# Optimization experiments

Measured on AMD Instinct MI355X. Metric: run time of the kernel, lower is better.

Reference implementation:

```python
import jax, jax.numpy as jnp
import numpy as np

B, IMGS, PH, PW = 4, 4, 16, 16      # 4 groups, 4 images/group, 16x16 patches per image
P, C = 16, 3
N = IMGS * PH * PW                   # 1024 packed tokens per group
PATCH_DIM = C * P * P                # 768
DIM, HEADS, DHEAD, DEPTH = 768, 12, 64, 4
INNER = HEADS * DHEAD
MLP = 3072
POSMAX = 32                          # image_size // patch_size
NCLS = 1000
SCALE = DHEAD ** 0.5


def _ln(x, g):
    # torch LayerNorm with learned gamma, beta frozen at 0
    mu = jnp.mean(x, -1, keepdims=True)
    var = jnp.var(x, -1, keepdims=True)
    return (x - mu) * jax.lax.rsqrt(var + 1e-5) * g


def _qk_rmsnorm(t, g):
    # F.normalize(t, dim=-1) * sqrt(dhead) * gamma[h, 1, d]; t: (b,h,n,d), g: (h,d)
    nrm = jnp.sqrt(jnp.sum(t * t, -1, keepdims=True))
    return t / jnp.maximum(nrm, 1e-12) * SCALE * g[None, :, None, :]


def _attention(x, context, ln_g, Wq, Wkv, qg, kg, Wo, attn_mask):
    xn = _ln(x, ln_g)
    kv_in = xn if context is None else context  # context is NOT normed (matches torch)
    q = xn @ Wq
    k, v = jnp.split(kv_in @ Wkv, 2, axis=-1)
    split = lambda t: t.reshape(t.shape[0], t.shape[1], HEADS, DHEAD).transpose(0, 2, 1, 3)
    q, k, v = split(q), split(k), split(v)
    q = _qk_rmsnorm(q, qg)
    k = _qk_rmsnorm(k, kg)
    dots = jnp.einsum('bhid,bhjd->bhij', q, k)  # no 1/sqrt(d): scale lives in RMSNorm
    dots = jnp.where(attn_mask, dots, -jnp.finfo(dots.dtype).max)
    attn = jax.nn.softmax(dots, axis=-1)
    out = jnp.einsum('bhij,bhjd->bhid', attn, v)
    out = out.transpose(0, 2, 1, 3).reshape(x.shape[0], -1, INNER)
    return out @ Wo


def _forward(patches, emb_ln_g, W_emb, b_emb, emb_ln2_g, pos_h, pos_w,
             ln_attn_g, Wq, Wkv, qn_g, kn_g, Wo,
             ln_ff_g, W1, b1, W2, b2, final_ln_g,
             pool_q, pool_ln_g, pWq, pWkv, p_qn_g, p_kn_g, pWo,
             head_ln_g, W_head,
             patch_positions, image_ids, lengths):
    valid = jnp.arange(N)[None, :] < lengths[:, None]              # (B,N) True = real token
    same_img = image_ids[:, :, None] == image_ids[:, None, :]      # (B,i,j) block-diagonal
    attn_mask = (same_img & valid[:, None, :])[:, None]            # (B,1,i,j)

    x = _ln(patches, emb_ln_g) @ W_emb + b_emb
    x = _ln(x, emb_ln2_g)
    x = x + pos_h[patch_positions[..., 0]] + pos_w[patch_positions[..., 1]]

    for l in range(DEPTH):
        x = _attention(x, None, ln_attn_g[l], Wq[l], Wkv[l], qn_g[l], kn_g[l], Wo[l], attn_mask) + x
        h = jax.nn.gelu(_ln(x, ln_ff_g[l]) @ W1[l] + b1[l], approximate=False)
        x = h @ W2[l] + b2[l] + x
    x = _ln(x, final_ln_g)

    # attention pooling: one learned query per packed image
    queries = jnp.broadcast_to(pool_q, (x.shape[0], IMGS, DIM))
    pool_mask = ((jnp.arange(IMGS)[None, :, None] == image_ids[:, None, :]) & valid[:, None, :])[:, None]
    pooled = _attention(queries, x, pool_ln_g, pWq, pWkv, p_qn_g, p_kn_g, pWo, pool_mask) + queries
    return _ln(pooled, head_ln_g) @ W_head  # (B, IMGS, NCLS), mlp_head has no bias


def setup_inputs():
    key = jax.random.key(0)
    ks = jax.random.split(key, 20)
    rn = lambda k, shape, s=0.02: (jax.random.normal(k, shape) * s).astype(jnp.float32)

    patches = jax.random.normal(ks[0], (B, N, PATCH_DIM), dtype=jnp.float32)
    hh, ww = jnp.meshgrid(jnp.arange(PH), jnp.arange(PW), indexing='ij')
    pos = jnp.stack([hh.reshape(-1), ww.reshape(-1)], axis=-1)        # (256,2)
    patch_positions = jnp.broadcast_to(jnp.tile(pos, (IMGS, 1))[None], (B, N, 2)).astype(jnp.int32)
    image_ids = jnp.broadcast_to(jnp.repeat(jnp.arange(IMGS), PH * PW)[None], (B, N)).astype(jnp.int32)
    lengths = jnp.full((B,), N, dtype=jnp.int32)

    return dict(
        patches=patches, patch_positions=patch_positions, image_ids=image_ids, lengths=lengths,
        emb_ln_g=jnp.ones(PATCH_DIM, jnp.float32), W_emb=rn(ks[1], (PATCH_DIM, DIM)),
        b_emb=jnp.zeros(DIM, jnp.float32), emb_ln2_g=jnp.ones(DIM, jnp.float32),
        pos_h=rn(ks[2], (POSMAX, DIM), 1.0), pos_w=rn(ks[3], (POSMAX, DIM), 1.0),
        ln_attn_g=jnp.ones((DEPTH, DIM), jnp.float32),
        Wq=rn(ks[4], (DEPTH, DIM, INNER)), Wkv=rn(ks[5], (DEPTH, DIM, 2 * INNER)),
        qn_g=jnp.ones((DEPTH, HEADS, DHEAD), jnp.float32), kn_g=jnp.ones((DEPTH, HEADS, DHEAD), jnp.float32),
        Wo=rn(ks[6], (DEPTH, INNER, DIM)),
        ln_ff_g=jnp.ones((DEPTH, DIM), jnp.float32),
        W1=rn(ks[7], (DEPTH, DIM, MLP)), b1=jnp.zeros((DEPTH, MLP), jnp.float32),
        W2=rn(ks[8], (DEPTH, MLP, DIM)), b2=jnp.zeros((DEPTH, DIM), jnp.float32),
        final_ln_g=jnp.ones(DIM, jnp.float32),
        pool_q=rn(ks[9], (DIM,), 1.0), pool_ln_g=jnp.ones(DIM, jnp.float32),
        pWq=rn(ks[10], (DIM, INNER)), pWkv=rn(ks[11], (DIM, 2 * INNER)),
        p_qn_g=jnp.ones((HEADS, DHEAD), jnp.float32), p_kn_g=jnp.ones((HEADS, DHEAD), jnp.float32),
        pWo=rn(ks[12], (INNER, DIM)),
        head_ln_g=jnp.ones(DIM, jnp.float32), W_head=rn(ks[13], (DIM, NCLS)),
    )


def reference(patches, patch_positions, image_ids, lengths,
              emb_ln_g, W_emb, b_emb, emb_ln2_g, pos_h, pos_w,
              ln_attn_g, Wq, Wkv, qn_g, kn_g, Wo,
              ln_ff_g, W1, b1, W2, b2, final_ln_g,
              pool_q, pool_ln_g, pWq, pWkv, p_qn_g, p_kn_g, pWo,
              head_ln_g, W_head):
    return _forward(patches, emb_ln_g, W_emb, b_emb, emb_ln2_g, pos_h, pos_w,
                    ln_attn_g, Wq, Wkv, qn_g, kn_g, Wo,
                    ln_ff_g, W1, b1, W2, b2, final_ln_g,
                    pool_q, pool_ln_g, pWq, pWkv, p_qn_g, p_kn_g, pWo,
                    head_ln_g, W_head, patch_positions, image_ids, lengths)
```

## Files before the change

### kernel.cpp

```cpp
#include <hip/hip_runtime.h>
#include <hip/hip_bf16.h>
#include <math.h>

using bf16 = __hip_bfloat16;
typedef short s16x8 __attribute__((ext_vector_type(8)));
typedef float f32x4 __attribute__((ext_vector_type(4)));

#define DEVI __device__ __forceinline__

static constexpr int NB    = 4;
static constexpr int NTOK  = 1024;
static constexpr int DIM   = 768;
static constexpr int NH    = 12;
static constexpr int MLPD  = 3072;
static constexpr int NLAYER= 4;
static constexpr int NIMG  = 4;
static constexpr int NCLS  = 1000;
static constexpr int MR    = NB * NTOK;

DEVI float b2f(bf16 v){ return __bfloat162float(v); }
DEVI bf16  f2b(float v){ return __float2bfloat16(v); }

DEVI void async16(const void* g, void* l) {
  __builtin_amdgcn_global_load_lds((const __attribute__((address_space(1))) void*)g,
                                   (__attribute__((address_space(3))) void*)l, 16, 0, 0);
}

DEVI f32x4 mfma16(s16x8 a, s16x8 b, f32x4 c) {
  return __builtin_amdgcn_mfma_f32_16x16x32_bf16(a, b, c, 0, 0, 0);
}

template<int N> DEVI void waitcnt_vm() {
  if constexpr (N == 0)      asm volatile("s_waitcnt vmcnt(0)" ::: "memory");
  else if constexpr (N == 4) asm volatile("s_waitcnt vmcnt(4)" ::: "memory");
  else if constexpr (N == 6) asm volatile("s_waitcnt vmcnt(6)" ::: "memory");
}

DEVI float block_sum(float v, float* scratch, int tid) {
  #pragma unroll
  for (int o = 32; o >= 1; o >>= 1) v += __shfl_xor(v, o);
  __syncthreads();
  if ((tid & 63) == 0) scratch[tid >> 6] = v;
  __syncthreads();
  return scratch[0] + scratch[1] + scratch[2] + scratch[3];
}

DEVI float block_max(float v, float* scratch, int tid) {
  #pragma unroll
  for (int o = 32; o >= 1; o >>= 1) v = fmaxf(v, __shfl_xor(v, o));
  __syncthreads();
  if ((tid & 63) == 0) scratch[tid >> 6] = v;
  __syncthreads();
  return fmaxf(fmaxf(scratch[0], scratch[1]), fmaxf(scratch[2], scratch[3]));
}

struct bh4 { bf16 a, b, c, d; };
struct TEntry { const float* src; bf16* dst; int R, C, tiles, tC; };
struct TDesc  { TEntry e[22]; };

__global__ __launch_bounds__(256) void transpose_kernel(TDesc D, int nent) {
  int bid = blockIdx.x, ei = 0;
  while (ei < nent - 1 && bid >= D.e[ei].tiles) { bid -= D.e[ei].tiles; ++ei; }
  const TEntry E = D.e[ei];
  const int tr = bid / E.tC, tc = bid % E.tC;
  __shared__ bf16 t[32][33];
  const int tid = threadIdx.x;
  const int lr = tid >> 3, lc = (tid & 7) * 4;
  const float* srow = E.src + (size_t)(tr*32 + lr)*E.C + tc*32 + lc;
  float4 v = *(const float4*)srow;
  t[lr][lc] = f2b(v.x); t[lr][lc+1] = f2b(v.y); t[lr][lc+2] = f2b(v.z); t[lr][lc+3] = f2b(v.w);
  __syncthreads();
  bh4 o;
  o.a = t[lc+0][lr]; o.b = t[lc+1][lr]; o.c = t[lc+2][lr]; o.d = t[lc+3][lr];
  *(bh4*)(E.dst + (size_t)(tc*32 + lr)*E.R + tr*32 + lc) = o;
}

__global__ __launch_bounds__(256) void ln768_kernel(const float* __restrict__ in,
    const float* __restrict__ g, bf16* __restrict__ out)
{
  __shared__ float scratch[4];
  const int row = blockIdx.x, tid = threadIdx.x;
  const float* p = in + (size_t)row*768;
  const float v0 = p[tid], v1 = p[tid+256], v2 = p[tid+512];
  const float s  = block_sum(v0+v1+v2, scratch, tid);
  const float ss = block_sum(v0*v0+v1*v1+v2*v2, scratch, tid);
  const float mu = s * (1.0f/768.0f);
  const float var = ss * (1.0f/768.0f) - mu*mu;
  const float rstd = rsqrtf(var + 1e-5f);
  bf16* o = out + (size_t)row*768;
  o[tid]     = f2b((v0-mu)*rstd*g[tid]);
  o[tid+256] = f2b((v1-mu)*rstd*g[tid+256]);
  o[tid+512] = f2b((v2-mu)*rstd*g[tid+512]);
}

__global__ __launch_bounds__(256) void ln_pos_kernel(const float* __restrict__ in,
    const float* __restrict__ g, const float* __restrict__ pos_h, const float* __restrict__ pos_w,
    const int* __restrict__ ppos, float* __restrict__ out)
{
  __shared__ float scratch[4];
  const int row = blockIdx.x, tid = threadIdx.x;
  const float* p = in + (size_t)row*768;
  const float v0 = p[tid], v1 = p[tid+256], v2 = p[tid+512];
  const float s  = block_sum(v0+v1+v2, scratch, tid);
  const float ss = block_sum(v0*v0+v1*v1+v2*v2, scratch, tid);
  const float mu = s * (1.0f/768.0f);
  const float rstd = rsqrtf(ss*(1.0f/768.0f) - mu*mu + 1e-5f);
  const int p0 = ppos[row*2], p1 = ppos[row*2+1];
  const float* ph = pos_h + (size_t)p0*768;
  const float* pw = pos_w + (size_t)p1*768;
  float* o = out + (size_t)row*768;
  o[tid]     = (v0-mu)*rstd*g[tid]     + ph[tid]     + pw[tid];
  o[tid+256] = (v1-mu)*rstd*g[tid+256] + ph[tid+256] + pw[tid+256];
  o[tid+512] = (v2-mu)*rstd*g[tid+512] + ph[tid+512] + pw[tid+512];
}

template<int DO_BIAS, int DO_GELU, int OUT_BF16, int DO_RES, int NTILE>
__global__ __launch_bounds__(256)
void gemm_mfma(const bf16* __restrict__ A, const bf16* __restrict__ BT,
               const float* __restrict__ bias, float* __restrict__ Cf,
               bf16* __restrict__ Cb, int M, int Nn, int K)
{
  constexpr int NF  = NTILE / 32;
  constexpr int PD  = (NTILE == 64) ? 4 : 3;
  constexpr int VW  = (NTILE == 64) ? 6 : 4;
  __shared__ bf16 As[PD][64*64];
  __shared__ bf16 Bs[PD][(NTILE/2)*64];
  const int tid = threadIdx.x;
  const int wid = tid >> 6, lane = tid & 63;
  const int quad = lane >> 4, l15 = lane & 15;
  const int wy = wid >> 1, wx = wid & 1;

  const int gx  = gridDim.x;
  const int nwg = gx * gridDim.y;
  const int bid = blockIdx.y * gx + blockIdx.x;
  const int qq  = nwg >> 3, rm = nwg & 7;
  const int xcd = bid & 7,  li = bid >> 3;
  const int swz = (xcd < rm ? xcd * (qq + 1) : rm * (qq + 1) + (xcd - rm) * qq) + li;
  const int m0 = (swz / gx) * 128, n0 = (swz % gx) * NTILE;

  const int rl = lane >> 3;
  const int cs = lane & 7;

  f32x4 acc[4][NF];
  #pragma unroll
  for (int i = 0; i < 4; ++i)
    #pragma unroll
    for (int j = 0; j < NF; ++j) acc[i][j] = (f32x4){0.f,0.f,0.f,0.f};

  auto stage = [&](int buf, int k0) {
    #pragma unroll
    for (int c = 0; c < 2; ++c) {
      const int rbase = wid*8 + c*32;
      const int r_abs = rbase + rl;
      const int ceff  = cs ^ (r_abs & 7);
      const int mg    = 2*r_abs + (ceff >> 2);
      const int jb    = (ceff & 3) * 16;
      async16((const char*)A + ((size_t)(m0 + mg)*K + k0)*2 + jb, (char*)As[buf] + rbase*128);
    }
    #pragma unroll
    for (int c = 0; c < NTILE/64; ++c) {
      const int rbase = wid*8 + c*32;
      const int r_abs = rbase + rl;
      const int ceff  = cs ^ (r_abs & 7);
      const int ng    = 2*r_abs + (ceff >> 2);
      const int jb    = (ceff & 3) * 16;
      async16((const char*)BT + ((size_t)(n0 + ng)*K + k0)*2 + jb, (char*)Bs[buf] + rbase*128);
    }
  };

  auto compute = [&](int cb) {
    s16x8 af[4], bfr[NF];
    #pragma unroll
    for (int mt = 0; mt < 4; ++mt) {
      const int m = wy*64 + mt*16 + l15;
      const int r = m >> 1;
      const int cq = (((m & 1) << 2) | quad) ^ (r & 7);
      af[mt] = *(const s16x8*)((const char*)As[cb] + r*128 + cq*16);
    }
    #pragma unroll
    for (int nt = 0; nt < NF; ++nt) {
      const int n = wx*(NTILE/2) + nt*16 + l15;
      const int r = n >> 1;
      const int cq = (((n & 1) << 2) | quad) ^ (r & 7);
      bfr[nt] = *(const s16x8*)((const char*)Bs[cb] + r*128 + cq*16);
    }
    #pragma unroll
    for (int mt = 0; mt < 4; ++mt)
      #pragma unroll
      for (int nt = 0; nt < NF; ++nt)
        acc[mt][nt] = mfma16(af[mt], bfr[nt], acc[mt][nt]);
  };

  const int nk = K >> 5;
  #pragma unroll
  for (int t = 0; t < PD - 1; ++t) stage(t, t << 5);

  int cbuf = 0, sbuf = PD - 1;
  const int mainN = nk - (PD - 1);
  for (int kt = 0; kt < mainN; ++kt) {
    __builtin_amdgcn_sched_barrier(0);
    waitcnt_vm<VW>();
    __builtin_amdgcn_s_barrier();
    __builtin_amdgcn_sched_barrier(0);
    stage(sbuf, (kt + PD - 1) << 5);
    compute(cbuf);
    cbuf = (cbuf + 1 == PD) ? 0 : cbuf + 1;
    sbuf = (sbuf + 1 == PD) ? 0 : sbuf + 1;
  }
  for (int kt = mainN; kt < nk; ++kt) {
    __builtin_amdgcn_sched_barrier(0);
    waitcnt_vm<0>();
    __builtin_amdgcn_s_barrier();
    __builtin_amdgcn_sched_barrier(0);
    compute(cbuf);
    cbuf = (cbuf + 1 == PD) ? 0 : cbuf + 1;
  }

  #pragma unroll
  for (int nt = 0; nt < NF; ++nt) {
    const int col = n0 + wx*(NTILE/2) + nt*16 + l15;
    float bv = 0.f;
    if constexpr (DO_BIAS) bv = bias[col];
    #pragma unroll
    for (int mt = 0; mt < 4; ++mt) {
      #pragma unroll
      for (int r = 0; r < 4; ++r) {
        const int row = m0 + wy*64 + mt*16 + quad*4 + r;
        float v = acc[mt][nt][r];
        if constexpr (DO_BIAS) v += bv;
        if constexpr (DO_GELU) v = 0.5f*v*(1.0f + erff(v*0.70710678118654752f));
        const size_t idx = (size_t)row*Nn + col;
        if constexpr (OUT_BF16) Cb[idx] = f2b(v);
        else if constexpr (DO_RES) Cf[idx] += v;
        else Cf[idx] = v;
      }
    }
  }
}

template<int IN_BF16, int DO_BIAS>
__global__ __launch_bounds__(256) void smallm_gemm(const void* __restrict__ Xv,
    const float* __restrict__ W, const float* __restrict__ bias,
    float* __restrict__ out, int Nn)
{
  __shared__ float Xs[16*768];
  __shared__ float red[4][16][64];
  const int tid = threadIdx.x;
  if constexpr (IN_BF16) {
    const bf16* X = (const bf16*)Xv;
    for (int i = tid; i < 16*768; i += 256) Xs[i] = b2f(X[i]);
  } else {
    const float* X = (const float*)Xv;
    for (int i = tid; i < 16*768; i += 256) Xs[i] = X[i];
  }
  __syncthreads();
  const int cl = tid & 63, kg = tid >> 6;
  const int c = blockIdx.x*64 + cl;
  float acc[16];
  #pragma unroll
  for (int r = 0; r < 16; ++r) acc[r] = 0.f;
  if (c < Nn) {
    const int k0 = kg*192;
    #pragma unroll 4
    for (int k = k0; k < k0 + 192; ++k) {
      const float w = W[(size_t)k*Nn + c];
      #pragma unroll
      for (int r = 0; r < 16; ++r) acc[r] += Xs[r*768 + k] * w;
    }
  }
  #pragma unroll
  for (int r = 0; r < 16; ++r) red[kg][r][cl] = acc[r];
  __syncthreads();
  if (kg == 0 && c < Nn) {
    #pragma unroll
    for (int r = 0; r < 16; ++r) {
      float v = red[0][r][cl] + red[1][r][cl] + red[2][r][cl] + red[3][r][cl];
      if constexpr (DO_BIAS) v += bias[c];
      out[(size_t)r*Nn + c] = v;
    }
  }
}

__global__ __launch_bounds__(256) void rms_qkv_kernel(const float* __restrict__ qkv,
    const float* __restrict__ qg, const float* __restrict__ kg,
    bf16* __restrict__ Qb, bf16* __restrict__ Kb, bf16* __restrict__ VTb)
{
  __shared__ float tile[64*68];
  const int nt = blockIdx.x, h = blockIdx.y, b = blockIdx.z;
  const int tid = threadIdx.x;
  const int bh = b*NH + h;
  const size_t rowbase = (size_t)(b*NTOK + nt*64);
  const int r = tid >> 2, pp = tid & 3;

  auto stage = [&](int off) {
    #pragma unroll
    for (int rr = 0; rr < 4; ++rr) {
      const int idx = rr*256 + tid;
      const int rw = idx >> 4, c4 = (idx & 15) << 2;
      float4 val = *(const float4*)(qkv + (rowbase + rw)*2304 + off + c4);
      *(float4*)(&tile[rw*68 + c4]) = val;
    }
  };

  stage(h*64);
  __syncthreads();
  {
    float ssq = 0.f;
    #pragma unroll
    for (int i = 0; i < 16; ++i) { float x = tile[r*68 + pp*16 + i]; ssq += x*x; }
    ssq += __shfl_xor(ssq, 1); ssq += __shfl_xor(ssq, 2);
    const float rn = 8.0f / fmaxf(sqrtf(ssq), 1e-12f);
    bf16* orow = Qb + ((size_t)bh*NTOK + nt*64 + r)*64;
    #pragma unroll
    for (int i = 0; i < 16; ++i) { int d = pp*16+i; orow[d] = f2b(tile[r*68+d]*rn*qg[h*64+d]); }
  }
  __syncthreads();
  stage(768 + h*64);
  __syncthreads();
  {
    float ssq = 0.f;
    #pragma unroll
    for (int i = 0; i < 16; ++i) { float x = tile[r*68 + pp*16 + i]; ssq += x*x; }
    ssq += __shfl_xor(ssq, 1); ssq += __shfl_xor(ssq, 2);
    const float rn = 8.0f / fmaxf(sqrtf(ssq), 1e-12f);
    bf16* orow = Kb + ((size_t)bh*NTOK + nt*64 + r)*64;
    #pragma unroll
    for (int i = 0; i < 16; ++i) { int d = pp*16+i; orow[d] = f2b(tile[r*68+d]*rn*kg[h*64+d]); }
  }
  __syncthreads();
  stage(1536 + h*64);
  __syncthreads();
  {
    const int d = tid >> 2;
    bf16* orow = VTb + ((size_t)bh*64 + d)*NTOK + nt*64;
    #pragma unroll
    for (int i = 0; i < 16; ++i) { int n = pp*16 + i; orow[n] = f2b(tile[n*68 + d]); }
  }
}

__global__ __launch_bounds__(256) void attn_mfma(const bf16* __restrict__ Qb,
    const bf16* __restrict__ Kb, const bf16* __restrict__ VTb, bf16* __restrict__ Ob,
    const int* __restrict__ ids, const int* __restrict__ lens)
{
  __shared__ bf16 Ps[4][16*72];
  __shared__ int  ids_s[NTOK];
  const int qt = blockIdx.x, h = blockIdx.y, b = blockIdx.z;
  const int tid = threadIdx.x;
  const int wid = tid >> 6, lane = tid & 63;
  const int quad = lane >> 4, l15 = lane & 15;
  const int bh = b*NH + h;
  const int q0 = qt*64;
  const int len = lens[b];

  #pragma unroll
  for (int i = 0; i < 4; ++i) ids_s[i*256 + tid] = ids[b*NTOK + i*256 + tid];
  __syncthreads();

  const bf16* qrow = Qb + ((size_t)bh*NTOK + q0 + wid*16 + l15)*64;
  const s16x8 aq0 = *(const s16x8*)(qrow + quad*8);
  const s16x8 aq1 = *(const s16x8*)(qrow + 32 + quad*8);

  int idq[4];
  #pragma unroll
  for (int rr = 0; rr < 4; ++rr) idq[rr] = ids_s[q0 + wid*16 + quad*4 + rr];

  unsigned qm = 0;
  #pragma unroll
  for (int rr = 0; rr < 4; ++rr) qm |= 1u << (idq[rr] & 31);
  #pragma unroll
  for (int o = 32; o >= 1; o >>= 1) qm |= (unsigned)__shfl_xor((int)qm, o);

  f32x4 oacc[4];
  #pragma unroll
  for (int nt = 0; nt < 4; ++nt) oacc[nt] = (f32x4){0.f,0.f,0.f,0.f};
  float mrow[4] = {-3.0e38f,-3.0e38f,-3.0e38f,-3.0e38f};
  float lrow[4] = {0.f,0.f,0.f,0.f};

  const bf16* Kgb = Kb  + (size_t)bh*NTOK*64;
  const bf16* Vgb = VTb + (size_t)bh*64*NTOK;
  bf16* pw = Ps[wid];

  for (int kt = 0; kt < 16; ++kt) {
    const int k0 = kt*64;
    const int idk_l = ids_s[k0 + lane];
    const bool ok = ((k0 + lane) < len) && (((qm >> (idk_l & 31)) & 1u) != 0u);
    if (__ballot(ok) == 0ULL) continue;

    f32x4 sA[4];
    #pragma unroll
    for (int jt = 0; jt < 4; ++jt) {
      const bf16* krow = Kgb + (size_t)(k0 + jt*16 + l15)*64;
      const s16x8 bk0 = *(const s16x8*)(krow + quad*8);
      const s16x8 bk1 = *(const s16x8*)(krow + 32 + quad*8);
      f32x4 s = (f32x4){0.f,0.f,0.f,0.f};
      s = mfma16(aq0, bk0, s);
      s = mfma16(aq1, bk1, s);
      sA[jt] = s;
    }
    #pragma unroll
    for (int jt = 0; jt < 4; ++jt) {
      const int j = k0 + jt*16 + l15;
      const int idk = ids_s[j];
      const bool kvld = j < len;
      #pragma unroll
      for (int rr = 0; rr < 4; ++rr)
        sA[jt][rr] = (kvld && idk == idq[rr]) ? sA[jt][rr] : -3.0e38f;
    }
    float alpha[4], mnew[4];
    #pragma unroll
    for (int rr = 0; rr < 4; ++rr) {
      float mx = fmaxf(fmaxf(sA[0][rr], sA[1][rr]), fmaxf(sA[2][rr], sA[3][rr]));
      mx = fmaxf(mx, __shfl_xor(mx, 1));
      mx = fmaxf(mx, __shfl_xor(mx, 2));
      mx = fmaxf(mx, __shfl_xor(mx, 4));
      mx = fmaxf(mx, __shfl_xor(mx, 8));
      const float mn = fmaxf(mrow[rr], mx);
      mnew[rr] = mn;
      alpha[rr] = expf(mrow[rr] - mn);
      mrow[rr] = mn;
    }
    #pragma unroll
    for (int rr = 0; rr < 4; ++rr) {
      float rs = 0.f;
      #pragma unroll
      for (int jt = 0; jt < 4; ++jt) {
        const float pv = (sA[jt][rr] > -1.0e38f) ? expf(sA[jt][rr] - mnew[rr]) : 0.0f;
        sA[jt][rr] = pv;
        rs += pv;
      }
      rs += __shfl_xor(rs, 1);
      rs += __shfl_xor(rs, 2);
      rs += __shfl_xor(rs, 4);
      rs += __shfl_xor(rs, 8);
      lrow[rr] = lrow[rr]*alpha[rr] + rs;
      #pragma unroll
      for (int nt = 0; nt < 4; ++nt) oacc[nt][rr] *= alpha[rr];
    }
    #pragma unroll
    for (int jt = 0; jt < 4; ++jt)
      #pragma unroll
      for (int rr = 0; rr < 4; ++rr)
        pw[(quad*4+rr)*72 + jt*16 + l15] = f2b(sA[jt][rr]);
    #pragma unroll
    for (int ss = 0; ss < 2; ++ss) {
      const s16x8 ap = *(const s16x8*)(pw + l15*72 + ss*32 + quad*8);
      #pragma unroll
      for (int nt = 0; nt < 4; ++nt) {
        const s16x8 bv = *(const s16x8*)(Vgb + (size_t)(nt*16 + l15)*NTOK + k0 + ss*32 + quad*8);
        oacc[nt] = mfma16(ap, bv, oacc[nt]);
      }
    }
  }

  #pragma unroll
  for (int rr = 0; rr < 4; ++rr) {
    const float inv = lrow[rr] > 0.f ? 1.0f/lrow[rr] : 0.0f;
    const int n = q0 + wid*16 + quad*4 + rr;
    bf16* orow = Ob + ((size_t)b*NTOK + n)*768 + h*64;
    #pragma unroll
    for (int nt = 0; nt < 4; ++nt)
      orow[nt*16 + l15] = f2b(oacc[nt][rr]*inv);
  }
}

__global__ __launch_bounds__(256) void pool_q_kernel(const float* __restrict__ pool_q,
    const float* __restrict__ pool_ln_g, const float* __restrict__ pWq,
    const float* __restrict__ p_qn_g, float* __restrict__ qp)
{
  __shared__ float xn[768];
  __shared__ float scratch[4];
  __shared__ float qraw[64];
  const int h = blockIdx.x, tid = threadIdx.x;
  float v0 = pool_q[tid], v1 = pool_q[tid+256], v2 = pool_q[tid+512];
  const float s  = block_sum(v0+v1+v2, scratch, tid);
  const float ss = block_sum(v0*v0+v1*v1+v2*v2, scratch, tid);
  const float mu = s*(1.0f/768.0f);
  const float rstd = rsqrtf(ss*(1.0f/768.0f) - mu*mu + 1e-5f);
  xn[tid]     = (v0-mu)*rstd*pool_ln_g[tid];
  xn[tid+256] = (v1-mu)*rstd*pool_ln_g[tid+256];
  xn[tid+512] = (v2-mu)*rstd*pool_ln_g[tid+512];
  __syncthreads();
  const int d = tid >> 2, pp = tid & 3;
  const int col = h*64 + d;
  float acc = 0.f;
  for (int k = pp*192; k < (pp+1)*192; ++k) acc += xn[k]*pWq[(size_t)k*768 + col];
  acc += __shfl_xor(acc, 1); acc += __shfl_xor(acc, 2);
  if (pp == 0) qraw[d] = acc;
  __syncthreads();
  if (tid < 64) {
    const float q = qraw[tid];
    float sq = q*q;
    #pragma unroll
    for (int o = 32; o >= 1; o >>= 1) sq += __shfl_xor(sq, o);
    const float rn = 8.0f / fmaxf(sqrtf(sq), 1e-12f);
    qp[h*64 + tid] = q * rn * p_qn_g[h*64 + tid];
  }
}

__global__ __launch_bounds__(256) void pool_attn_kernel(const float* __restrict__ kvp,
    const float* __restrict__ qp, const float* __restrict__ kg,
    const int* __restrict__ ids, const int* __restrict__ lens, float* __restrict__ pooled)
{
  __shared__ float sp[1024];
  __shared__ float qg_s[64];
  __shared__ float scratch[4];
  __shared__ float outred[4][64];
  const int h = blockIdx.x, img = blockIdx.y, b = blockIdx.z;
  const int tid = threadIdx.x;
  const int len = lens[b];
  if (tid < 64) qg_s[tid] = qp[h*64 + tid] * kg[h*64 + tid];
  __syncthreads();

  float smax = -3.0e38f;
  for (int j = tid; j < 1024; j += 256) {
    float sv = -3.0e38f;
    if (j < len && ids[b*NTOK + j] == img) {
      const float* kr = kvp + (size_t)(b*NTOK + j)*1536 + h*64;
      float ssq = 0.f, dq = 0.f;
      #pragma unroll
      for (int dd = 0; dd < 64; dd += 4) {
        float4 k4 = *(const float4*)(kr + dd);
        ssq += k4.x*k4.x + k4.y*k4.y + k4.z*k4.z + k4.w*k4.w;
        dq  += qg_s[dd]*k4.x + qg_s[dd+1]*k4.y + qg_s[dd+2]*k4.z + qg_s[dd+3]*k4.w;
      }
      const float rn = 8.0f / fmaxf(sqrtf(ssq), 1e-12f);
      sv = dq * rn;
    }
    sp[j] = sv;
    smax = fmaxf(smax, sv);
  }
  const float M = block_max(smax, scratch, tid);
  float lsum = 0.f;
  for (int j = tid; j < 1024; j += 256) {
    const float p = (sp[j] > -1.0e38f) ? expf(sp[j] - M) : 0.0f;
    sp[j] = p;
    lsum += p;
  }
  const float L = block_sum(lsum, scratch, tid);
  const float invL = L > 0.f ? 1.0f / L : 0.0f;

  const int d = tid & 63, jg = tid >> 6;
  float acc = 0.f;
  for (int j = jg; j < 1024; j += 4) {
    const float p = sp[j];
    if (p > 0.f) acc += p * kvp[(size_t)(b*NTOK + j)*1536 + 768 + h*64 + d];
  }
  outred[jg][d] = acc;
  __syncthreads();
  if (tid < 64) {
    const float o = (outred[0][tid] + outred[1][tid] + outred[2][tid] + outred[3][tid]) * invL;
    pooled[((size_t)b*NIMG + img)*768 + h*64 + tid] = o;
  }
}

extern "C" void kernel_launch(void* const* d_in, const int* in_sizes, int n_in,
                              void* d_out, int out_size, void* d_ws, size_t ws_size,
                              hipStream_t stream)
{
  const float* patches    = (const float*)d_in[0];
  const int*   ppos       = (const int*)d_in[1];
  const int*   image_ids  = (const int*)d_in[2];
  const int*   lengths    = (const int*)d_in[3];
  const float* emb_ln_g   = (const float*)d_in[4];
  const float* W_emb      = (const float*)d_in[5];
  const float* b_emb      = (const float*)d_in[6];
  const float* emb_ln2_g  = (const float*)d_in[7];
  const float* pos_h      = (const float*)d_in[8];
  const float* pos_w      = (const float*)d_in[9];
  const float* ln_attn_g  = (const float*)d_in[10];
  const float* Wq         = (const float*)d_in[11];
  const float* Wkv        = (const float*)d_in[12];
  const float* qn_g       = (const float*)d_in[13];
  const float* kn_g       = (const float*)d_in[14];
  const float* Wo         = (const float*)d_in[15];
  const float* ln_ff_g    = (const float*)d_in[16];
  const float* W1         = (const float*)d_in[17];
  const float* b1         = (const float*)d_in[18];
  const float* W2         = (const float*)d_in[19];
  const float* b2v        = (const float*)d_in[20];
  const float* final_ln_g = (const float*)d_in[21];
  const float* pool_q     = (const float*)d_in[22];
  const float* pool_ln_g  = (const float*)d_in[23];
  const float* pWq        = (const float*)d_in[24];
  const float* pWkv       = (const float*)d_in[25];
  const float* p_qn_g     = (const float*)d_in[26];
  const float* p_kn_g     = (const float*)d_in[27];
  const float* pWo        = (const float*)d_in[28];
  const float* head_ln_g  = (const float*)d_in[29];
  const float* W_head     = (const float*)d_in[30];

  char* ws = (char*)d_ws;
  size_t off = 0;
  auto alloc = [&](size_t sz){ size_t r = off; off += (sz + 255) & ~(size_t)255; return r; };

  const size_t o_WembT = alloc((size_t)768*768*2);
  size_t o_QKVT[4], o_WoT[4], o_W1T[4], o_W2T[4];
  for (int l = 0; l < NLAYER; ++l) {
    o_QKVT[l] = alloc((size_t)2304*768*2);
    o_WoT[l]  = alloc((size_t)768*768*2);
    o_W1T[l]  = alloc((size_t)3072*768*2);
    o_W2T[l]  = alloc((size_t)768*3072*2);
  }
  const size_t o_pWkvT = alloc((size_t)1536*768*2);
  const size_t o_x     = alloc((size_t)MR*768*4);
  const size_t o_xn    = alloc((size_t)MR*768*2);
  const size_t o_qkv   = alloc((size_t)MR*2304*4);
  const size_t o_Qb    = alloc((size_t)MR*768*2);
  const size_t o_Kb    = alloc((size_t)MR*768*2);
  const size_t o_VT    = alloc((size_t)MR*768*2);
  const size_t o_Ob    = alloc((size_t)MR*768*2);
  const size_t o_qp    = alloc((size_t)768*4);
  const size_t o_pool  = alloc((size_t)16*768*4);
  const size_t o_poolf = alloc((size_t)16*768*4);
  const size_t o_hl    = alloc((size_t)16*768*2);
  if (off > ws_size) return;

  float* x    = (float*)(ws + o_x);
  bf16*  xn   = (bf16*)(ws + o_xn);
  float* qkv  = (float*)(ws + o_qkv);
  bf16*  hb   = (bf16*)(ws + o_qkv);
  bf16*  Qb   = (bf16*)(ws + o_Qb);
  bf16*  Kb   = (bf16*)(ws + o_Kb);
  bf16*  VTb  = (bf16*)(ws + o_VT);
  bf16*  Ob   = (bf16*)(ws + o_Ob);
  float* qp   = (float*)(ws + o_qp);
  float* pooled  = (float*)(ws + o_pool);
  float* pooledf = (float*)(ws + o_poolf);
  bf16*  hl   = (bf16*)(ws + o_hl);

  TDesc td; int ne = 0, total = 0;
  auto add = [&](const float* s, size_t dofs, int R, int C){
    td.e[ne].src = s;
    td.e[ne].dst = (bf16*)(ws + dofs);
    td.e[ne].R = R; td.e[ne].C = C;
    td.e[ne].tiles = (R/32)*(C/32); td.e[ne].tC = C/32;
    total += td.e[ne].tiles; ++ne;
  };
  add(W_emb, o_WembT, 768, 768);
  for (int l = 0; l < NLAYER; ++l) {
    add(Wq  + (size_t)l*768*768,  o_QKVT[l],                 768, 768);
    add(Wkv + (size_t)l*768*1536, o_QKVT[l] + (size_t)768*768*2, 768, 1536);
    add(Wo  + (size_t)l*768*768,  o_WoT[l],                  768, 768);
    add(W1  + (size_t)l*768*3072, o_W1T[l],                  768, 3072);
    add(W2  + (size_t)l*3072*768, o_W2T[l],                  3072, 768);
  }
  add(pWkv, o_pWkvT, 768, 1536);
  transpose_kernel<<<total, 256, 0, stream>>>(td, ne);

  ln768_kernel<<<MR, 256, 0, stream>>>(patches, emb_ln_g, xn);
  gemm_mfma<1,0,0,0,64><<<dim3(12,32), 256, 0, stream>>>(xn, (const bf16*)(ws+o_WembT), b_emb,
                                                         qkv, nullptr, MR, 768, 768);
  ln_pos_kernel<<<MR, 256, 0, stream>>>(qkv, emb_ln2_g, pos_h, pos_w, ppos, x);

  for (int l = 0; l < NLAYER; ++l) {
    ln768_kernel<<<MR, 256, 0, stream>>>(x, ln_attn_g + (size_t)l*768, xn);
    gemm_mfma<0,0,0,0,128><<<dim3(18,32), 256, 0, stream>>>(xn, (const bf16*)(ws+o_QKVT[l]), nullptr,
                                                            qkv, nullptr, MR, 2304, 768);
    rms_qkv_kernel<<<dim3(16,NH,NB), 256, 0, stream>>>(qkv, qn_g + (size_t)l*768, kn_g + (size_t)l*768,
                                                       Qb, Kb, VTb);
    attn_mfma<<<dim3(16,NH,NB), 256, 0, stream>>>(Qb, Kb, VTb, Ob, image_ids, lengths);
    gemm_mfma<0,0,0,1,64><<<dim3(12,32), 256, 0, stream>>>(Ob, (const bf16*)(ws+o_WoT[l]), nullptr,
                                                           x, nullptr, MR, 768, 768);
    ln768_kernel<<<MR, 256, 0, stream>>>(x, ln_ff_g + (size_t)l*768, xn);
    gemm_mfma<1,1,1,0,128><<<dim3(24,32), 256, 0, stream>>>(xn, (const bf16*)(ws+o_W1T[l]), b1 + (size_t)l*3072,
                                                            nullptr, hb, MR, 3072, 768);
    gemm_mfma<1,0,0,1,64><<<dim3(12,32), 256, 0, stream>>>(hb, (const bf16*)(ws+o_W2T[l]), b2v + (size_t)l*768,
                                                           x, nullptr, MR, 768, 3072);
  }

  ln768_kernel<<<MR, 256, 0, stream>>>(x, final_ln_g, xn);
  gemm_mfma<0,0,0,0,128><<<dim3(12,32), 256, 0, stream>>>(xn, (const bf16*)(ws+o_pWkvT), nullptr,
                                                          qkv, nullptr, MR, 1536, 768);
  pool_q_kernel<<<NH, 256, 0, stream>>>(pool_q, pool_ln_g, pWq, p_qn_g, qp);
  pool_attn_kernel<<<dim3(NH,NIMG,NB), 256, 0, stream>>>(qkv, qp, p_kn_g, image_ids, lengths, pooled);
  smallm_gemm<0,1><<<12, 256, 0, stream>>>(pooled, pWo, pool_q, pooledf, 768);
  ln768_kernel<<<16, 256, 0, stream>>>(pooledf, head_ln_g, hl);
  smallm_gemm<1,0><<<16, 256, 0, stream>>>(hl, W_head, nullptr, (float*)d_out, NCLS);
}
```

Baseline: 1.148 ms.

## Split-K narrow GEMMs into partial slabs and fuse reduction with residual+LayerNorm

```diff
diff --git a/kernel.cpp b/kernel.cpp
--- a/kernel.cpp
+++ b/kernel.cpp
@@ -17,6 +17,7 @@
 static constexpr int NIMG  = 4;
 static constexpr int NCLS  = 1000;
 static constexpr int MR    = NB * NTOK;
+static constexpr size_t SLAB = (size_t)MR * 768;
 
 DEVI float b2f(bf16 v){ return __bfloat162float(v); }
 DEVI bf16  f2b(float v){ return __float2bfloat16(v); }
@@ -32,6 +33,7 @@
 
 template<int N> DEVI void waitcnt_vm() {
   if constexpr (N == 0)      asm volatile("s_waitcnt vmcnt(0)" ::: "memory");
+  else if constexpr (N == 3) asm volatile("s_waitcnt vmcnt(3)" ::: "memory");
   else if constexpr (N == 4) asm volatile("s_waitcnt vmcnt(4)" ::: "memory");
   else if constexpr (N == 6) asm volatile("s_waitcnt vmcnt(6)" ::: "memory");
 }
@@ -93,36 +95,79 @@
   o[tid+512] = f2b((v2-mu)*rstd*g[tid+512]);
 }
 
-__global__ __launch_bounds__(256) void ln_pos_kernel(const float* __restrict__ in,
-    const float* __restrict__ g, const float* __restrict__ pos_h, const float* __restrict__ pos_w,
-    const int* __restrict__ ppos, float* __restrict__ out)
+template<int HAS_BIAS>
+__global__ __launch_bounds__(256) void res2_ln_kernel(float* __restrict__ x,
+    const float* __restrict__ P, const float* __restrict__ bias,
+    const float* __restrict__ g, bf16* __restrict__ xn)
 {
   __shared__ float scratch[4];
   const int row = blockIdx.x, tid = threadIdx.x;
-  const float* p = in + (size_t)row*768;
-  const float v0 = p[tid], v1 = p[tid+256], v2 = p[tid+512];
-  const float s  = block_sum(v0+v1+v2, scratch, tid);
-  const float ss = block_sum(v0*v0+v1*v1+v2*v2, scratch, tid);
+  const size_t base = (size_t)row*768;
+  const float* p0 = P + base;
+  const float* p1 = P + SLAB + base;
+  float* xr = x + base;
+  float v[3];
+  #pragma unroll
+  for (int i = 0; i < 3; ++i) {
+    const int c = tid + i*256;
+    float t = xr[c] + p0[c] + p1[c];
+    if constexpr (HAS_BIAS) t += bias[c];
+    v[i] = t;
+    xr[c] = t;
+  }
+  const float s  = block_sum(v[0]+v[1]+v[2], scratch, tid);
+  const float ss = block_sum(v[0]*v[0]+v[1]*v[1]+v[2]*v[2], scratch, tid);
   const float mu = s * (1.0f/768.0f);
   const float rstd = rsqrtf(ss*(1.0f/768.0f) - mu*mu + 1e-5f);
-  const int p0 = ppos[row*2], p1 = ppos[row*2+1];
-  const float* ph = pos_h + (size_t)p0*768;
-  const float* pw = pos_w + (size_t)p1*768;
-  float* o = out + (size_t)row*768;
-  o[tid]     = (v0-mu)*rstd*g[tid]     + ph[tid]     + pw[tid];
-  o[tid+256] = (v1-mu)*rstd*g[tid+256] + ph[tid+256] + pw[tid+256];
-  o[tid+512] = (v2-mu)*rstd*g[tid+512] + ph[tid+512] + pw[tid+512];
-}
-
-template<int DO_BIAS, int DO_GELU, int OUT_BF16, int DO_RES, int NTILE>
+  bf16* o = xn + base;
+  #pragma unroll
+  for (int i = 0; i < 3; ++i) {
+    const int c = tid + i*256;
+    o[c] = f2b((v[i]-mu)*rstd*g[c]);
+  }
+}
+
+__global__ __launch_bounds__(256) void ln_pos2_kernel(const float* __restrict__ P,
+    const float* __restrict__ bias, const float* __restrict__ g,
+    const float* __restrict__ pos_h, const float* __restrict__ pos_w,
+    const int* __restrict__ ppos, float* __restrict__ out)
+{
+  __shared__ float scratch[4];
+  const int row = blockIdx.x, tid = threadIdx.x;
+  const size_t base = (size_t)row*768;
+  const float* p0 = P + base;
+  const float* p1 = P + SLAB + base;
+  float v[3];
+  #pragma unroll
+  for (int i = 0; i < 3; ++i) {
+    const int c = tid + i*256;
+    v[i] = p0[c] + p1[c] + bias[c];
+  }
+  const float s  = block_sum(v[0]+v[1]+v[2], scratch, tid);
+  const float ss = block_sum(v[0]*v[0]+v[1]*v[1]+v[2]*v[2], scratch, tid);
+  const float mu = s * (1.0f/768.0f);
+  const float rstd = rsqrtf(ss*(1.0f/768.0f) - mu*mu + 1e-5f);
+  const int p0i = ppos[row*2], p1i = ppos[row*2+1];
+  const float* ph = pos_h + (size_t)p0i*768;
+  const float* pw = pos_w + (size_t)p1i*768;
+  float* o = out + base;
+  #pragma unroll
+  for (int i = 0; i < 3; ++i) {
+    const int c = tid + i*256;
+    o[c] = (v[i]-mu)*rstd*g[c] + ph[c] + pw[c];
+  }
+}
+
+template<int DO_BIAS, int DO_GELU, int OUT_BF16, int DO_RES, int NTILE, int SPLITK>
 __global__ __launch_bounds__(256)
 void gemm_mfma(const bf16* __restrict__ A, const bf16* __restrict__ BT,
                const float* __restrict__ bias, float* __restrict__ Cf,
                bf16* __restrict__ Cb, int M, int Nn, int K)
 {
   constexpr int NF  = NTILE / 32;
-  constexpr int PD  = (NTILE == 64) ? 4 : 3;
-  constexpr int VW  = (NTILE == 64) ? 6 : 4;
+  constexpr int PD  = 3;
+  constexpr int LPI = 2 + NTILE/64;
+  constexpr int VW  = (PD - 2) * LPI;
   __shared__ bf16 As[PD][64*64];
   __shared__ bf16 Bs[PD][(NTILE/2)*64];
   const int tid = threadIdx.x;
@@ -138,6 +183,10 @@
   const int swz = (xcd < rm ? xcd * (qq + 1) : rm * (qq + 1) + (xcd - rm) * qq) + li;
   const int m0 = (swz / gx) * 128, n0 = (swz % gx) * NTILE;
 
+  const int kz    = (SPLITK > 1) ? blockIdx.z : 0;
+  const int kloc  = K / SPLITK;
+  const int kbase = kz * kloc;
+
   const int rl = lane >> 3;
   const int cs = lane & 7;
 
@@ -191,9 +240,9 @@
         acc[mt][nt] = mfma16(af[mt], bfr[nt], acc[mt][nt]);
   };
 
-  const int nk = K >> 5;
-  #pragma unroll
-  for (int t = 0; t < PD - 1; ++t) stage(t, t << 5);
+  const int nk = kloc >> 5;
+  #pragma unroll
+  for (int t = 0; t < PD - 1; ++t) stage(t, kbase + (t << 5));
 
   int cbuf = 0, sbuf = PD - 1;
   const int mainN = nk - (PD - 1);
@@ -202,7 +251,7 @@
     waitcnt_vm<VW>();
     __builtin_amdgcn_s_barrier();
     __builtin_amdgcn_sched_barrier(0);
-    stage(sbuf, (kt + PD - 1) << 5);
+    stage(sbuf, kbase + ((kt + PD - 1) << 5));
     compute(cbuf);
     cbuf = (cbuf + 1 == PD) ? 0 : cbuf + 1;
     sbuf = (sbuf + 1 == PD) ? 0 : sbuf + 1;
@@ -216,6 +265,7 @@
     cbuf = (cbuf + 1 == PD) ? 0 : cbuf + 1;
   }
 
+  float* Cslab = (SPLITK > 1) ? (Cf + (size_t)kz * SLAB) : Cf;
   #pragma unroll
   for (int nt = 0; nt < NF; ++nt) {
     const int col = n0 + wx*(NTILE/2) + nt*16 + l15;
@@ -231,8 +281,8 @@
         if constexpr (DO_GELU) v = 0.5f*v*(1.0f + erff(v*0.70710678118654752f));
         const size_t idx = (size_t)row*Nn + col;
         if constexpr (OUT_BF16) Cb[idx] = f2b(v);
-        else if constexpr (DO_RES) Cf[idx] += v;
-        else Cf[idx] = v;
+        else if constexpr (DO_RES) Cslab[idx] += v;
+        else Cslab[idx] = v;
       }
     }
   }
@@ -605,6 +655,7 @@
   const size_t o_x     = alloc((size_t)MR*768*4);
   const size_t o_xn    = alloc((size_t)MR*768*2);
   const size_t o_qkv   = alloc((size_t)MR*2304*4);
+  const size_t o_P     = alloc((size_t)2*SLAB*4);
   const size_t o_Qb    = alloc((size_t)MR*768*2);
   const size_t o_Kb    = alloc((size_t)MR*768*2);
   const size_t o_VT    = alloc((size_t)MR*768*2);
@@ -619,6 +670,7 @@
   bf16*  xn   = (bf16*)(ws + o_xn);
   float* qkv  = (float*)(ws + o_qkv);
   bf16*  hb   = (bf16*)(ws + o_qkv);
+  float* P    = (float*)(ws + o_P);
   bf16*  Qb   = (bf16*)(ws + o_Qb);
   bf16*  Kb   = (bf16*)(ws + o_Kb);
   bf16*  VTb  = (bf16*)(ws + o_VT);
@@ -648,29 +700,30 @@
   transpose_kernel<<<total, 256, 0, stream>>>(td, ne);
 
   ln768_kernel<<<MR, 256, 0, stream>>>(patches, emb_ln_g, xn);
-  gemm_mfma<1,0,0,0,64><<<dim3(12,32), 256, 0, stream>>>(xn, (const bf16*)(ws+o_WembT), b_emb,
-                                                         qkv, nullptr, MR, 768, 768);
-  ln_pos_kernel<<<MR, 256, 0, stream>>>(qkv, emb_ln2_g, pos_h, pos_w, ppos, x);
+  gemm_mfma<0,0,0,0,64,2><<<dim3(12,32,2), 256, 0, stream>>>(xn, (const bf16*)(ws+o_WembT), nullptr,
+                                                             P, nullptr, MR, 768, 768);
+  ln_pos2_kernel<<<MR, 256, 0, stream>>>(P, b_emb, emb_ln2_g, pos_h, pos_w, ppos, x);
+  ln768_kernel<<<MR, 256, 0, stream>>>(x, ln_attn_g, xn);
 
   for (int l = 0; l < NLAYER; ++l) {
-    ln768_kernel<<<MR, 256, 0, stream>>>(x, ln_attn_g + (size_t)l*768, xn);
-    gemm_mfma<0,0,0,0,128><<<dim3(18,32), 256, 0, stream>>>(xn, (const bf16*)(ws+o_QKVT[l]), nullptr,
-                                                            qkv, nullptr, MR, 2304, 768);
+    gemm_mfma<0,0,0,0,64,1><<<dim3(36,32), 256, 0, stream>>>(xn, (const bf16*)(ws+o_QKVT[l]), nullptr,
+                                                             qkv, nullptr, MR, 2304, 768);
     rms_qkv_kernel<<<dim3(16,NH,NB), 256, 0, stream>>>(qkv, qn_g + (size_t)l*768, kn_g + (size_t)l*768,
                                                        Qb, Kb, VTb);
     attn_mfma<<<dim3(16,NH,NB), 256, 0, stream>>>(Qb, Kb, VTb, Ob, image_ids, lengths);
-    gemm_mfma<0,0,0,1,64><<<dim3(12,32), 256, 0, stream>>>(Ob, (const bf16*)(ws+o_WoT[l]), nullptr,
-                                                           x, nullptr, MR, 768, 768);
-    ln768_kernel<<<MR, 256, 0, stream>>>(x, ln_ff_g + (size_t)l*768, xn);
-    gemm_mfma<1,1,1,0,128><<<dim3(24,32), 256, 0, stream>>>(xn, (const bf16*)(ws+o_W1T[l]), b1 + (size_t)l*3072,
-                                                            nullptr, hb, MR, 3072, 768);
-    gemm_mfma<1,0,0,1,64><<<dim3(12,32), 256, 0, stream>>>(hb, (const bf16*)(ws+o_W2T[l]), b2v + (size_t)l*768,
-                                                           x, nullptr, MR, 768, 3072);
-  }
-
-  ln768_kernel<<<MR, 256, 0, stream>>>(x, final_ln_g, xn);
-  gemm_mfma<0,0,0,0,128><<<dim3(12,32), 256, 0, stream>>>(xn, (const bf16*)(ws+o_pWkvT), nullptr,
-                                                          qkv, nullptr, MR, 1536, 768);
+    gemm_mfma<0,0,0,0,64,2><<<dim3(12,32,2), 256, 0, stream>>>(Ob, (const bf16*)(ws+o_WoT[l]), nullptr,
+                                                               P, nullptr, MR, 768, 768);
+    res2_ln_kernel<0><<<MR, 256, 0, stream>>>(x, P, nullptr, ln_ff_g + (size_t)l*768, xn);
+    gemm_mfma<1,1,1,0,128,1><<<dim3(24,32), 256, 0, stream>>>(xn, (const bf16*)(ws+o_W1T[l]), b1 + (size_t)l*3072,
+                                                              nullptr, hb, MR, 3072, 768);
+    gemm_mfma<0,0,0,0,64,2><<<dim3(12,32,2), 256, 0, stream>>>(hb, (const bf16*)(ws+o_W2T[l]), nullptr,
+                                                               P, nullptr, MR, 768, 3072);
+    const float* gnext = (l + 1 < NLAYER) ? (ln_attn_g + (size_t)(l+1)*768) : final_ln_g;
+    res2_ln_kernel<1><<<MR, 256, 0, stream>>>(x, P, b2v + (size_t)l*768, gnext, xn);
+  }
+
+  gemm_mfma<0,0,0,0,64,1><<<dim3(24,32), 256, 0, stream>>>(xn, (const bf16*)(ws+o_pWkvT), nullptr,
+                                                           qkv, nullptr, MR, 1536, 768);
   pool_q_kernel<<<NH, 256, 0, stream>>>(pool_q, pool_ln_g, pWq, p_qn_g, qp);
   pool_attn_kernel<<<dim3(NH,NIMG,NB), 256, 0, stream>>>(qkv, qp, p_kn_g, image_ids, lengths, pooled);
   smallm_gemm<0,1><<<12, 256, 0, stream>>>(pooled, pWo, pool_q, pooledf, 768);
```

Result: faster. 1.122 ms (-2.2%).
